# Optimization experiments

Measured on AMD Instinct MI355X. Metric: run time of the kernel, lower is better.

## Reference

```python
import jax, jax.numpy as jnp
import numpy as np

B, L, D = 4, 4096, 1024


def hippo_freqs(dim):
    n = np.arange(dim, dtype=np.float32)
    f = np.sqrt(2 * n + 1)
    f = f / f.max()
    return np.exp(-f * np.log(10000)).astype(np.float32)


def setup_inputs() -> dict:
    key = jax.random.key(0)
    ks = jax.random.split(key, 8)
    s = 1.0 / np.sqrt(D)
    return {
        "x": jax.random.normal(ks[0], (B, L, D), dtype=jnp.float32),
        "omega": jnp.asarray(hippo_freqs(D)),
        "log_gamma": jax.random.normal(ks[1], (D,), dtype=jnp.float32) - 3.0,
        "dt": jnp.float32(0.1),
        "W_psi": jax.random.uniform(ks[2], (2 * D, D), jnp.float32, -s, s),
        "b_psi": jax.random.uniform(ks[3], (2 * D,), jnp.float32, -s, s),
        "W_phi": jax.random.uniform(ks[4], (2 * D, D), jnp.float32, -s, s),
        "b_phi": jax.random.uniform(ks[5], (2 * D,), jnp.float32, -s, s),
        "W_gate": jax.random.uniform(ks[6], (D, D), jnp.float32, -s, s),
        "b_gate": jax.random.uniform(ks[7], (D,), jnp.float32, -s, s),
    }


def _proj(z):
    # exact_projection: per-channel-axis standardization over last dim (biased var)
    mean = z.mean(axis=-1, keepdims=True)
    var = ((z - mean) ** 2).mean(axis=-1, keepdims=True)
    return (z - mean) / (jnp.sqrt(var) + 1e-6)


def reference(x, omega, log_gamma, dt, W_psi, b_psi, W_phi, b_phi, W_gate, b_gate):
    Bn, Ln, Dn = x.shape
    psi_raw = jnp.einsum("bld,ed->ble", x, W_psi) + b_psi
    phi_raw = jnp.einsum("bld,ed->ble", x, W_phi) + b_phi
    psi = jax.lax.complex(psi_raw[..., :Dn], psi_raw[..., Dn:])
    phi = jax.lax.complex(phi_raw[..., :Dn], phi_raw[..., Dn:])
    gate = jax.nn.sigmoid(jnp.einsum("bld,ed->ble", x, W_gate) + b_gate)
    U = gate.astype(psi.dtype) * psi  # [B,L,D] complex

    dt_abs = jnp.abs(dt)
    lam = jax.lax.complex(-jnp.exp(log_gamma), omega)  # [D]
    t_axis = jnp.arange(Ln, dtype=jnp.float32)
    kernel = jnp.exp(lam[None, :] * t_axis[:, None].astype(lam.dtype) * dt_abs)  # [L,D]

    n_fft = 2 * Ln
    Kf = jnp.fft.fft(kernel, n=n_fft, axis=0)          # [2L,D]
    Uf = jnp.fft.fft(U, n=n_fft, axis=1)               # [B,2L,D]
    H = jnp.fft.ifft(Uf * Kf[None], axis=1)[:, :Ln]    # causal conv, [B,L,D]

    H_proj = jax.lax.complex(_proj(H.real), _proj(H.imag))
    return (H_proj * jnp.conj(phi)).real
```

## Files before the change

kernel.cpp:

```cpp
#include <hip/hip_runtime.h>
#include <hip/hip_bf16.h>
#include <math.h>

#define B_ 4
#define L_ 4096
#define D_ 1024
#define M_ (B_*L_)
#define N_ 5120
#define K_ 1024
#define CHUNKS 256
#define LC 16
#define PL ((long)M_ * D_)

#define WS_NEEDED 211812352ull

typedef __attribute__((ext_vector_type(8))) short bf16x8;
typedef __attribute__((ext_vector_type(4))) float f32x4;
typedef __attribute__((ext_vector_type(4))) unsigned short u16x4;

__device__ inline float b2f(short s) {
    unsigned u = ((unsigned)(unsigned short)s) << 16;
    float f; __builtin_memcpy(&f, &u, 4); return f;
}
__device__ inline unsigned short f2bu(float f) {
    __hip_bfloat16 h = __float2bfloat16(f);
    unsigned short u; __builtin_memcpy(&u, &h, 2); return u;
}

__device__ inline void cvt4(const float4* __restrict__ src, ushort* __restrict__ dst, long j) {
    float4 v = src[j];
    __hip_bfloat16 a = __float2bfloat16(v.x), b = __float2bfloat16(v.y),
                   c = __float2bfloat16(v.z), d = __float2bfloat16(v.w);
    ushort4 o = { *(ushort*)&a, *(ushort*)&b, *(ushort*)&c, *(ushort*)&d };
    *(ushort4*)(dst + j * 4) = o;
}

__global__ void convert_kernel(const float* __restrict__ x,
                               const float* __restrict__ Wpsi,
                               const float* __restrict__ Wphi,
                               const float* __restrict__ Wgate,
                               ushort* __restrict__ xb,
                               ushort* __restrict__ wb) {
    long i0 = (long)blockIdx.x * blockDim.x + threadIdx.x;
    long stride = (long)gridDim.x * blockDim.x;
    const long nx4 = ((long)M_ * K_) >> 2;
    for (long j = i0; j < nx4; j += stride) cvt4((const float4*)x, xb, j);
    const long nW14 = (2048L * 1024) >> 2, nW34 = (1024L * 1024) >> 2;
    for (long j = i0; j < nW14; j += stride) cvt4((const float4*)Wpsi, wb, j);
    for (long j = i0; j < nW14; j += stride) cvt4((const float4*)Wphi, wb + 2048L * 1024, j);
    for (long j = i0; j < nW34; j += stride) cvt4((const float4*)Wgate, wb + 4096L * 1024, j);
}

#define BM2 256
#define BN2 256
#define BK2 64
#define NT  (K_ / BK2)
#define DBUF_BYTES 65536

#define STAGE(gptr, brow, kt, slotoff)                                                       \
  do {                                                                                       \
    const __hip_bfloat16* g0_ = (gptr) + (long)((brow) + srow0) * K_ + (kt) * 64 + sgc0 * 8; \
    const __hip_bfloat16* g1_ = (gptr) + (long)((brow) + srow1) * K_ + (kt) * 64 + sgc1 * 8; \
    __builtin_amdgcn_global_load_lds((const __attribute__((address_space(1))) void*)g0_,     \
        (__attribute__((address_space(3))) void*)(smem + (slotoff) + ldst0), 16, 0, 0);      \
    __builtin_amdgcn_global_load_lds((const __attribute__((address_space(1))) void*)g1_,     \
        (__attribute__((address_space(3))) void*)(smem + (slotoff) + ldst1), 16, 0, 0);      \
  } while (0)

#define RDA1(db, qm, i_)                                                            \
  do {                                                                              \
    aA[i_][0] = *(const bf16x8*)((db) + aoff + (qm) * 8192 + (i_) * 2048 + ct0);    \
    aA[i_][1] = *(const bf16x8*)((db) + aoff + (qm) * 8192 + (i_) * 2048 + ct1);    \
  } while (0)
#define RDB1(db, qn, s, j_)                                                         \
  do {                                                                              \
    bB[s][j_][0] = *(const bf16x8*)((db) + boff + (qn) * 4096 + (j_) * 2048 + ct0); \
    bB[s][j_][1] = *(const bf16x8*)((db) + boff + (qn) * 4096 + (j_) * 2048 + ct1); \
  } while (0)

#define MFMA16(qm, qn, s)                                                                         \
  _Pragma("unroll") for (int i_ = 0; i_ < 4; ++i_)                                                \
    _Pragma("unroll") for (int j_ = 0; j_ < 2; ++j_) {                                            \
      acc[(qm)*4+i_][(qn)*2+j_] = __builtin_amdgcn_mfma_f32_16x16x32_bf16(                        \
          aA[i_][0], bB[s][j_][0], acc[(qm)*4+i_][(qn)*2+j_], 0, 0, 0);                           \
      acc[(qm)*4+i_][(qn)*2+j_] = __builtin_amdgcn_mfma_f32_16x16x32_bf16(                        \
          aA[i_][1], bB[s][j_][1], acc[(qm)*4+i_][(qn)*2+j_], 0, 0, 0);                           \
    }
#define BARRIER __builtin_amdgcn_s_barrier()

#define COMPUTE_TILE(db)                                                                          \
  do {                                                                                            \
    RDA1(db, 0, 0); RDB1(db, 0, 0, 0); RDB1(db, 0, 0, 1);                                         \
    RDA1(db, 0, 1); RDA1(db, 0, 2); RDA1(db, 0, 3);                                               \
    __builtin_amdgcn_s_setprio(1); MFMA16(0, 0, 0); __builtin_amdgcn_s_setprio(0);                \
    RDB1(db, 1, 1, 0); RDB1(db, 1, 1, 1);                                                         \
    __builtin_amdgcn_s_setprio(1); MFMA16(0, 1, 1); __builtin_amdgcn_s_setprio(0);                \
    RDA1(db, 1, 0); RDA1(db, 1, 1); RDA1(db, 1, 2); RDA1(db, 1, 3);                               \
    __builtin_amdgcn_s_setprio(1); MFMA16(1, 1, 1); MFMA16(1, 0, 0);                              \
    __builtin_amdgcn_s_setprio(0);                                                                \
  } while (0)

__global__ __launch_bounds__(512, 2)
void gemm_kernel(const __hip_bfloat16* __restrict__ xb,
                 const __hip_bfloat16* __restrict__ wb,
                 const float* __restrict__ b_psi,
                 const float* __restrict__ b_phi,
                 const float* __restrict__ b_gate,
                 __hip_bfloat16* __restrict__ raw5) {
    __shared__ __attribute__((aligned(16))) char smem[2 * DBUF_BYTES];

    const int tid   = threadIdx.x;
    const int wid   = tid >> 6;
    const int lane  = tid & 63;
    const int row16 = lane & 15;
    const int quad  = lane >> 4;
    const int wm    = wid >> 2;
    const int wn    = wid & 3;

    const int bid = blockIdx.y * 64 + blockIdx.x;
    const int swz = (bid & 7) * (1280 / 8) + (bid >> 3);
    const int m_blk = (swz & 63) * BM2;
    const int n_blk = (swz >> 6) * BN2;

    const int srow0 = tid >> 3;
    const int srow1 = (512 + tid) >> 3;
    const int sch   = tid & 7;
    const int sgc0  = sch ^ (srow0 & 7);
    const int sgc1  = sch ^ (srow1 & 7);
    const int ldst0 = (wid * 64) * 16;
    const int ldst1 = (512 + wid * 64) * 16;

    const int sw   = row16 & 7;
    const int aoff = wm * 16384 + row16 * 128;
    const int boff = 32768 + (wn >> 1) * 16384 + ((wn & 1) * 64 + row16) * 128;
    const int ct0  = ((0 * 4 + quad) ^ sw) * 16;
    const int ct1  = ((1 * 4 + quad) ^ sw) * 16;

    bf16x8 aA[4][2];
    bf16x8 bB[2][2][2];
    f32x4  acc[8][4] = {};

    STAGE(xb, m_blk,       0, 0);
    STAGE(xb, m_blk + 128, 0, 16384);
    STAGE(wb, n_blk,       0, 32768);
    STAGE(wb, n_blk + 128, 0, 32768 + 16384);
    asm volatile("s_waitcnt vmcnt(0)" ::: "memory");
    BARRIER;

    for (int t = 0; t < NT - 1; ++t) {
        char* db = smem + (t & 1) * DBUF_BYTES;
        const int nb = ((t + 1) & 1) * DBUF_BYTES;
        STAGE(xb, m_blk,       t + 1, nb);
        STAGE(xb, m_blk + 128, t + 1, nb + 16384);
        STAGE(wb, n_blk,       t + 1, nb + 32768);
        STAGE(wb, n_blk + 128, t + 1, nb + 32768 + 16384);
        COMPUTE_TILE(db);
        asm volatile("s_waitcnt vmcnt(0)" ::: "memory");
        BARRIER;
    }
    {
        char* db = smem + ((NT - 1) & 1) * DBUF_BYTES;
        COMPUTE_TILE(db);
    }

#pragma unroll
    for (int mi = 0; mi < 8; ++mi) {
        const int mbase = m_blk + wm * 128 + (mi >> 2) * 64 + (mi & 3) * 16 + quad * 4;
#pragma unroll
        for (int nj = 0; nj < 4; ++nj) {
            int n = n_blk + wn * 64 + (nj >> 1) * 32 + (nj & 1) * 16 + row16;
            float bias = (n < 2048) ? b_psi[n] : (n < 4096) ? b_phi[n - 2048] : b_gate[n - 4096];
            int g = n >> 10, d = n & 1023;
            __hip_bfloat16* pl = raw5 + (long)g * PL;
#pragma unroll
            for (int r = 0; r < 4; ++r)
                pl[(long)(mbase + r) * D_ + d] = __float2bfloat16(acc[mi][nj][r] + bias);
        }
    }
}

__global__ __launch_bounds__(256) void scan1_kernel(__hip_bfloat16* raw5,
                                                    const float2* __restrict__ apow,
                                                    float2* __restrict__ E) {
    const int d0 = threadIdx.x * 4;
    const int c  = blockIdx.x;
    const int b  = blockIdx.y;

    float ar[4], ai[4];
#pragma unroll
    for (int q = 0; q < 4; ++q) {
        float2 a = apow[d0 + q];
        ar[q] = a.x; ai[q] = a.y;
    }

    ushort* Pre = (ushort*)raw5;
    ushort* Pim = (ushort*)(raw5 + PL);
    const ushort* Gt = (const ushort*)(raw5 + 4 * PL);
    long base = (long)(b * L_ + c * LC) * D_ + d0;

    float hr[4] = {0.f, 0.f, 0.f, 0.f}, hi[4] = {0.f, 0.f, 0.f, 0.f};
    for (int i = 0; i < LC; i++) {
        long idx = base + (long)i * D_;
        u16x4 pr = *(const u16x4*)(Pre + idx);
        u16x4 pi = *(const u16x4*)(Pim + idx);
        u16x4 gt = *(const u16x4*)(Gt + idx);
        u16x4 orr, oii;
#pragma unroll
        for (int q = 0; q < 4; ++q) {
            float sg = 1.f / (1.f + expf(-b2f((short)gt[q])));
            float ur = sg * b2f((short)pr[q]);
            float ui = sg * b2f((short)pi[q]);
            float nr = ar[q] * hr[q] - ai[q] * hi[q] + ur;
            float ni = ar[q] * hi[q] + ai[q] * hr[q] + ui;
            hr[q] = nr; hi[q] = ni;
            orr[q] = f2bu(nr);
            oii[q] = f2bu(ni);
        }
        *(u16x4*)(Pre + idx) = orr;
        *(u16x4*)(Pim + idx) = oii;
    }
    float2* Eo = E + ((long)c * B_ + b) * D_ + d0;
#pragma unroll
    for (int q = 0; q < 4; ++q) Eo[q] = make_float2(hr[q], hi[q]);
}

__global__ void apow_kernel(const float* __restrict__ omega,
                            const float* __restrict__ log_gamma,
                            const float* __restrict__ dtp,
                            float2* __restrict__ apow) {
    int t = blockIdx.x * blockDim.x + threadIdx.x;
    int i = t >> 10, d = t & 1023;
    float dt = fabsf(dtp[0]);
    float e = expf(-expf(log_gamma[d]) * dt * (float)(i + 1));
    float ang = omega[d] * dt * (float)(i + 1);
    apow[t] = make_float2(e * cosf(ang), e * sinf(ang));
}

__global__ __launch_bounds__(256) void carry_kernel(const float2* __restrict__ E,
                                                    const float* __restrict__ omega,
                                                    const float* __restrict__ log_gamma,
                                                    const float* __restrict__ dtp,
                                                    float2* __restrict__ carry) {
    const int g = blockIdx.x * 256 + threadIdx.x;
    const int b = g >> 10, d = g & 1023;
    const float dt = fabsf(dtp[0]);
    const float T = dt * (float)LC;
    const float dec = expf(-expf(log_gamma[d]) * T);
    const float ang = omega[d] * T;
    const float Ar = dec * cosf(ang), Ai = dec * sinf(ang);

    float tr = 0.f, ti = 0.f;
#pragma unroll 4
    for (int c = 0; c < CHUNKS; ++c) {
        const long idx = ((long)c * B_ + b) * D_ + d;
        carry[idx] = make_float2(tr, ti);
        float2 e = E[idx];
        float nr = e.x + Ar * tr - Ai * ti;
        float ni = e.y + Ar * ti + Ai * tr;
        tr = nr; ti = ni;
    }
}

__global__ __launch_bounds__(256) void finish_kernel(const __hip_bfloat16* __restrict__ raw5,
                                                     const float2* __restrict__ carry,
                                                     const float2* __restrict__ apow,
                                                     float* __restrict__ out) {
    const int wv = threadIdx.x >> 6, lane = threadIdx.x & 63;
    const int r = blockIdx.x * 4 + wv;
    const int l = r & (L_ - 1);
    const int b = r >> 12;
    const int c = l >> 4, i = l & (LC - 1);
    const int d0 = lane * 16;
    const long base = (long)r * D_ + d0;

    const __hip_bfloat16* Hre = raw5;
    const __hip_bfloat16* Him = raw5 + PL;
    const __hip_bfloat16* Pre = raw5 + 2 * PL;
    const __hip_bfloat16* Pim = raw5 + 3 * PL;
    const float2* cr = carry + ((long)c * B_ + b) * D_ + d0;
    const float2* ap = apow + (long)i * D_ + d0;

    bf16x8 hre[2], him[2];
    hre[0] = *(const bf16x8*)(Hre + base);     hre[1] = *(const bf16x8*)(Hre + base + 8);
    him[0] = *(const bf16x8*)(Him + base);     him[1] = *(const bf16x8*)(Him + base + 8);

    float hr[16], hi[16];
    float s0 = 0.f, s1 = 0.f, s2 = 0.f, s3 = 0.f;
#pragma unroll
    for (int j = 0; j < 16; j++) {
        float2 cv = cr[j];
        float2 av = ap[j];
        float fr = av.x * cv.x - av.y * cv.y;
        float fi = av.x * cv.y + av.y * cv.x;
        float xr = b2f(hre[j >> 3][j & 7]) + fr;
        float xi = b2f(him[j >> 3][j & 7]) + fi;
        hr[j] = xr; hi[j] = xi;
        s0 += xr; s1 += xr * xr; s2 += xi; s3 += xi * xi;
    }
#pragma unroll
    for (int m = 1; m < 64; m <<= 1) {
        s0 += __shfl_xor(s0, m);
        s1 += __shfl_xor(s1, m);
        s2 += __shfl_xor(s2, m);
        s3 += __shfl_xor(s3, m);
    }
    float mean_r = s0 * (1.f / D_);
    float var_r  = s1 * (1.f / D_) - mean_r * mean_r;
    float mean_i = s2 * (1.f / D_);
    float var_i  = s3 * (1.f / D_) - mean_i * mean_i;
    float inv_r = 1.f / (sqrtf(fmaxf(var_r, 0.f)) + 1e-6f);
    float inv_i = 1.f / (sqrtf(fmaxf(var_i, 0.f)) + 1e-6f);

    bf16x8 pre[2], pim[2];
    pre[0] = *(const bf16x8*)(Pre + base);     pre[1] = *(const bf16x8*)(Pre + base + 8);
    pim[0] = *(const bf16x8*)(Pim + base);     pim[1] = *(const bf16x8*)(Pim + base + 8);

    float o[16];
#pragma unroll
    for (int j = 0; j < 16; j++)
        o[j] = (hr[j] - mean_r) * inv_r * b2f(pre[j >> 3][j & 7])
             + (hi[j] - mean_i) * inv_i * b2f(pim[j >> 3][j & 7]);
#pragma unroll
    for (int q = 0; q < 4; q++)
        *(float4*)(out + base + q * 4) = make_float4(o[q*4], o[q*4+1], o[q*4+2], o[q*4+3]);
}

extern "C" void kernel_launch(void* const* d_in, const int* in_sizes, int n_in,
                              void* d_out, int out_size, void* d_ws, size_t ws_size,
                              hipStream_t stream) {
    (void)in_sizes; (void)n_in; (void)out_size;
    if (ws_size < WS_NEEDED) return;

    const float* x         = (const float*)d_in[0];
    const float* omega     = (const float*)d_in[1];
    const float* log_gamma = (const float*)d_in[2];
    const float* dt        = (const float*)d_in[3];
    const float* W_psi     = (const float*)d_in[4];
    const float* b_psi     = (const float*)d_in[5];
    const float* W_phi     = (const float*)d_in[6];
    const float* b_phi     = (const float*)d_in[7];
    const float* W_gate    = (const float*)d_in[8];
    const float* b_gate    = (const float*)d_in[9];

    char* ws = (char*)d_ws;
    __hip_bfloat16* xb   = (__hip_bfloat16*)(ws);
    __hip_bfloat16* wb   = (__hip_bfloat16*)(ws + 33554432);
    __hip_bfloat16* raw5 = (__hip_bfloat16*)(ws + 44040192);
    float2* E     = (float2*)(ws);
    float2* carry = (float2*)(ws + 8388608);
    float2* apow  = (float2*)(ws + 16777216);
    float* out = (float*)d_out;

    convert_kernel<<<2048, 256, 0, stream>>>(x, W_psi, W_phi, W_gate, (ushort*)xb, (ushort*)wb);
    gemm_kernel<<<dim3(M_ / BM2, N_ / BN2), 512, 0, stream>>>(xb, wb, b_psi, b_phi, b_gate, raw5);
    apow_kernel<<<(LC * D_) / 256, 256, 0, stream>>>(omega, log_gamma, dt, apow);
    scan1_kernel<<<dim3(CHUNKS, B_), 256, 0, stream>>>(raw5, apow, E);
    carry_kernel<<<(B_ * D_) / 256, 256, 0, stream>>>(E, omega, log_gamma, dt, carry);
    finish_kernel<<<M_ / 4, 256, 0, stream>>>(raw5, carry, apow, out);
}
```

Measured before the change: 447.7 us.

## Restructure GEMM main loop into k-half LDS slots with fine-grained prefetch

Replaces the 128KB double-buffered LDS pipeline with a single 64KB buffer split into two k-halves (32 columns each). Global-to-LDS loads for the next tile are issued into a half as soon as its readers pass a barrier, with partial vmcnt waits. This lowers LDS use per block so more blocks can be resident, and overlaps loads with MFMA at finer granularity. In exchange it adds more barriers per iteration and uses a new swizzle layout, which risks stalls or bank conflicts.

```diff
diff --git a/kernel.cpp b/kernel.cpp
--- a/kernel.cpp
+++ b/kernel.cpp
@@ -55,50 +55,33 @@
 #define BN2 256
 #define BK2 64
 #define NT  (K_ / BK2)
-#define DBUF_BYTES 65536
-
-#define STAGE(gptr, brow, kt, slotoff)                                                       \
-  do {                                                                                       \
-    const __hip_bfloat16* g0_ = (gptr) + (long)((brow) + srow0) * K_ + (kt) * 64 + sgc0 * 8; \
-    const __hip_bfloat16* g1_ = (gptr) + (long)((brow) + srow1) * K_ + (kt) * 64 + sgc1 * 8; \
-    __builtin_amdgcn_global_load_lds((const __attribute__((address_space(1))) void*)g0_,     \
-        (__attribute__((address_space(3))) void*)(smem + (slotoff) + ldst0), 16, 0, 0);      \
-    __builtin_amdgcn_global_load_lds((const __attribute__((address_space(1))) void*)g1_,     \
-        (__attribute__((address_space(3))) void*)(smem + (slotoff) + ldst1), 16, 0, 0);      \
+
+#define GLOAD(src, dstoff)                                                                  \
+    __builtin_amdgcn_global_load_lds((const __attribute__((address_space(1))) void*)(src),  \
+        (__attribute__((address_space(3))) void*)(smem + (dstoff)), 16, 0, 0)
+
+#define STG(gp, koff, slot)                                                                 \
+  do {                                                                                      \
+    GLOAD((gp) + (koff),            (slot) + sd0);                                          \
+    GLOAD((gp) + 128 * K_ + (koff), (slot) + sd1);                                          \
   } while (0)
 
-#define RDA1(db, qm, i_)                                                            \
-  do {                                                                              \
-    aA[i_][0] = *(const bf16x8*)((db) + aoff + (qm) * 8192 + (i_) * 2048 + ct0);    \
-    aA[i_][1] = *(const bf16x8*)((db) + aoff + (qm) * 8192 + (i_) * 2048 + ct1);    \
-  } while (0)
-#define RDB1(db, qn, s, j_)                                                         \
-  do {                                                                              \
-    bB[s][j_][0] = *(const bf16x8*)((db) + boff + (qn) * 4096 + (j_) * 2048 + ct0); \
-    bB[s][j_][1] = *(const bf16x8*)((db) + boff + (qn) * 4096 + (j_) * 2048 + ct1); \
-  } while (0)
-
-#define MFMA16(qm, qn, s)                                                                         \
-  _Pragma("unroll") for (int i_ = 0; i_ < 4; ++i_)                                                \
-    _Pragma("unroll") for (int j_ = 0; j_ < 2; ++j_) {                                            \
-      acc[(qm)*4+i_][(qn)*2+j_] = __builtin_amdgcn_mfma_f32_16x16x32_bf16(                        \
-          aA[i_][0], bB[s][j_][0], acc[(qm)*4+i_][(qn)*2+j_], 0, 0, 0);                           \
-      acc[(qm)*4+i_][(qn)*2+j_] = __builtin_amdgcn_mfma_f32_16x16x32_bf16(                        \
-          aA[i_][1], bB[s][j_][1], acc[(qm)*4+i_][(qn)*2+j_], 0, 0, 0);                           \
-    }
+#define RA(dst, kh, qm)                                                                     \
+  _Pragma("unroll") for (int i_ = 0; i_ < 4; ++i_)                                          \
+    dst[i_] = *(const bf16x8*)(smem + (kh) * 16384 + abase + ((qm) * 64 + i_ * 16) * 64);
+#define RB(dst, kh, s)                                                                      \
+  _Pragma("unroll") for (int j_ = 0; j_ < 2; ++j_)                                          \
+    dst[j_] = *(const bf16x8*)(smem + (kh) * 16384 + bbase + ((s) * 32 + j_ * 16) * 64);
+
+#define MM8(qm, s, av, bv)                                                                  \
+  _Pragma("unroll") for (int i_ = 0; i_ < 4; ++i_)                                          \
+    _Pragma("unroll") for (int j_ = 0; j_ < 2; ++j_)                                        \
+      acc[(qm)*4+i_][(s)*2+j_] = __builtin_amdgcn_mfma_f32_16x16x32_bf16(                   \
+          av[i_], bv[j_], acc[(qm)*4+i_][(s)*2+j_], 0, 0, 0);
+
 #define BARRIER __builtin_amdgcn_s_barrier()
-
-#define COMPUTE_TILE(db)                                                                          \
-  do {                                                                                            \
-    RDA1(db, 0, 0); RDB1(db, 0, 0, 0); RDB1(db, 0, 0, 1);                                         \
-    RDA1(db, 0, 1); RDA1(db, 0, 2); RDA1(db, 0, 3);                                               \
-    __builtin_amdgcn_s_setprio(1); MFMA16(0, 0, 0); __builtin_amdgcn_s_setprio(0);                \
-    RDB1(db, 1, 1, 0); RDB1(db, 1, 1, 1);                                                         \
-    __builtin_amdgcn_s_setprio(1); MFMA16(0, 1, 1); __builtin_amdgcn_s_setprio(0);                \
-    RDA1(db, 1, 0); RDA1(db, 1, 1); RDA1(db, 1, 2); RDA1(db, 1, 3);                               \
-    __builtin_amdgcn_s_setprio(1); MFMA16(1, 1, 1); MFMA16(1, 0, 0);                              \
-    __builtin_amdgcn_s_setprio(0);                                                                \
-  } while (0)
+#define PRIO1 __builtin_amdgcn_s_setprio(1)
+#define PRIO0 __builtin_amdgcn_s_setprio(0)
 
 __global__ __launch_bounds__(512, 2)
 void gemm_kernel(const __hip_bfloat16* __restrict__ xb,
@@ -107,7 +90,7 @@
                  const float* __restrict__ b_phi,
                  const float* __restrict__ b_gate,
                  __hip_bfloat16* __restrict__ raw5) {
-    __shared__ __attribute__((aligned(16))) char smem[2 * DBUF_BYTES];
+    __shared__ __attribute__((aligned(16))) char smem[65536];
 
     const int tid   = threadIdx.x;
     const int wid   = tid >> 6;
@@ -122,45 +105,57 @@
     const int m_blk = (swz & 63) * BM2;
     const int n_blk = (swz >> 6) * BN2;
 
-    const int srow0 = tid >> 3;
-    const int srow1 = (512 + tid) >> 3;
-    const int sch   = tid & 7;
-    const int sgc0  = sch ^ (srow0 & 7);
-    const int sgc1  = sch ^ (srow1 & 7);
-    const int ldst0 = (wid * 64) * 16;
-    const int ldst1 = (512 + wid * 64) * 16;
-
-    const int sw   = row16 & 7;
-    const int aoff = wm * 16384 + row16 * 128;
-    const int boff = 32768 + (wn >> 1) * 16384 + ((wn & 1) * 64 + row16) * 128;
-    const int ct0  = ((0 * 4 + quad) ^ sw) * 16;
-    const int ct1  = ((1 * 4 + quad) ^ sw) * 16;
-
-    bf16x8 aA[4][2];
-    bf16x8 bB[2][2][2];
+    const int cposq = ((quad ^ ((row16 >> 1) & 3)) * 16);
+    const int abase = (wm * 128 + row16) * 64 + cposq;
+    const int bbase = 32768 + (wn * 64 + row16) * 64 + cposq;
+
+    const int grow = tid >> 2;
+    const int gc   = (tid & 3) ^ ((tid >> 3) & 3);
+    const __hip_bfloat16* gA = xb + (long)(m_blk + grow) * K_ + gc * 8;
+    const __hip_bfloat16* gB = wb + (long)(n_blk + grow) * K_ + gc * 8;
+    const int sd0 = wid * 1024;
+    const int sd1 = 8192 + wid * 1024;
+    char* const sA0 = smem;
+    char* const sA1 = smem + 16384;
+    char* const sB0 = smem + 32768;
+    char* const sB1 = smem + 49152;
+
+    bf16x8 a[4], a2[4], b0[2], b1[2];
     f32x4  acc[8][4] = {};
 
-    STAGE(xb, m_blk,       0, 0);
-    STAGE(xb, m_blk + 128, 0, 16384);
-    STAGE(wb, n_blk,       0, 32768);
-    STAGE(wb, n_blk + 128, 0, 32768 + 16384);
-    asm volatile("s_waitcnt vmcnt(0)" ::: "memory");
+    STG(gA, 0,  (long)(sA0 - smem));
+    STG(gB, 0,  (long)(sB0 - smem));
+    STG(gA, 32, (long)(sA1 - smem));
+    STG(gB, 32, (long)(sB1 - smem));
+    asm volatile("s_waitcnt vmcnt(4)" ::: "memory");
     BARRIER;
 
-    for (int t = 0; t < NT - 1; ++t) {
-        char* db = smem + (t & 1) * DBUF_BYTES;
-        const int nb = ((t + 1) & 1) * DBUF_BYTES;
-        STAGE(xb, m_blk,       t + 1, nb);
-        STAGE(xb, m_blk + 128, t + 1, nb + 16384);
-        STAGE(wb, n_blk,       t + 1, nb + 32768);
-        STAGE(wb, n_blk + 128, t + 1, nb + 32768 + 16384);
-        COMPUTE_TILE(db);
-        asm volatile("s_waitcnt vmcnt(0)" ::: "memory");
-        BARRIER;
-    }
-    {
-        char* db = smem + ((NT - 1) & 1) * DBUF_BYTES;
-        COMPUTE_TILE(db);
+    for (int t = 0; t < NT; ++t) {
+        const bool pf = (t + 1 < NT);
+        const int kn = (t + 1) * 64;
+        RA(a, 0, 0); RB(b0, 0, 0); RB(b1, 0, 1);
+        PRIO1; MM8(0, 0, a, b0); MM8(0, 1, a, b1); PRIO0;
+        BARRIER;
+        if (pf) STG(gB, kn, 32768);
+        RA(a2, 0, 1);
+        PRIO1; MM8(1, 1, a2, b1); PRIO0;
+        BARRIER;
+        if (pf) STG(gA, kn, 0);
+        PRIO1; MM8(1, 0, a2, b0); PRIO0;
+        if (pf) { asm volatile("s_waitcnt vmcnt(4)" ::: "memory"); }
+        else    { asm volatile("s_waitcnt vmcnt(0)" ::: "memory"); }
+        BARRIER;
+        RA(a, 1, 0); RB(b0, 1, 0); RB(b1, 1, 1);
+        PRIO1; MM8(0, 0, a, b0); MM8(0, 1, a, b1); PRIO0;
+        BARRIER;
+        if (pf) STG(gB, kn + 32, 49152);
+        RA(a2, 1, 1);
+        PRIO1; MM8(1, 1, a2, b1); PRIO0;
+        BARRIER;
+        if (pf) STG(gA, kn + 32, 16384);
+        PRIO1; MM8(1, 0, a2, b0); PRIO0;
+        asm volatile("s_waitcnt vmcnt(4)" ::: "memory");
+        BARRIER;
     }
 
 #pragma unroll
```

Result: no change. 451.6 us (+0.9%).
